# Optimization experiments

Hardware: AMD Instinct MI355X
Metric: run time of the kernel (lower is better)

## Reference

```python
import jax, jax.numpy as jnp
import numpy as np

N = 50000
E = 1600000
H = 64  # hidden_dim
NEG_SLOPE = 0.2  # PyG GATConv default


def _gat(x, src, dst, W, a_s, a_d, b, n):
    """Single-head PyG GATConv (heads=1, concat=True, add_self_loops applied by caller)."""
    h = x @ W                                   # [N, d_out]
    e = jax.nn.leaky_relu(h[src] @ a_s + h[dst] @ a_d, NEG_SLOPE)  # [E']
    # segment softmax over edges grouped by destination node
    m = jax.ops.segment_max(e, dst, num_segments=n)                # [N]
    ex = jnp.exp(e - m[dst])
    denom = jax.ops.segment_sum(ex, dst, num_segments=n)           # [N]
    alpha = ex / denom[dst]                                        # [E']
    out = jax.ops.segment_sum(alpha[:, None] * h[src], dst, num_segments=n)
    return out + b


def setup_inputs() -> dict:
    key = jax.random.key(0)
    ks = jax.random.split(key, 16)
    x = jax.random.normal(ks[0], (N, 1), jnp.float32)
    edge_index = jax.random.randint(ks[1], (2, E), 0, N, dtype=jnp.int32)
    edge_attr = jax.random.normal(ks[2], (E, 1), jnp.float32)  # unused by module

    def lin(k, fi, fo):
        return jax.random.normal(k, (fi, fo), jnp.float32) * (1.0 / np.sqrt(fi))

    def att(k, fo):
        return jax.random.normal(k, (fo,), jnp.float32) * (1.0 / np.sqrt(fo))

    return {
        "x": x, "edge_index": edge_index, "edge_attr": edge_attr,
        "W1": lin(ks[3], 1, H),  "as1": att(ks[4], H),  "ad1": att(ks[5], H),  "b1": jnp.zeros((H,), jnp.float32),
        "W2": lin(ks[6], H, H),  "as2": att(ks[7], H),  "ad2": att(ks[8], H),  "b2": jnp.zeros((H,), jnp.float32),
        "W3": lin(ks[9], H, 1),  "as3": att(ks[10], 1), "ad3": att(ks[11], 1), "b3": jnp.zeros((1,), jnp.float32),
    }


def reference(x, edge_index, edge_attr, W1, as1, ad1, b1, W2, as2, ad2, b2, W3, as3, ad3, b3):
    n = x.shape[0]
    # GATConv default add_self_loops=True
    loops = jnp.arange(n, dtype=edge_index.dtype)
    src = jnp.concatenate([edge_index[0], loops])
    dst = jnp.concatenate([edge_index[1], loops])
    h = jax.nn.relu(_gat(x, src, dst, W1, as1, ad1, b1, n))
    h = jax.nn.relu(_gat(h, src, dst, W2, as2, ad2, b2, n))
    out = _gat(h, src, dst, W3, as3, ad3, b3, n)
    return out.squeeze(-1)  # [N]
```

## Files before the change

### kernel.cpp

```cpp
#include <hip/hip_runtime.h>

#define NEG_SLOPE 0.2f
#define BSH 8
#define BSZ 256
#define SC_PT 16
#define SC_CHUNK (256 * SC_PT)
#define STAGE_MAX 24576
#define GH 256

__device__ __forceinline__ float leaky(float v) { return v > 0.f ? v : NEG_SLOPE * v; }
__device__ __forceinline__ float rdlane(float v, int l) {
    return __uint_as_float(__builtin_amdgcn_readlane(__float_as_uint(v), l));
}


__global__ void k_bhist(const int* __restrict__ dst, int E, int* __restrict__ parts) {
    __shared__ int h[256];
    int tid = threadIdx.x;
    h[tid] = 0;
    __syncthreads();
    for (int i = blockIdx.x * 256 + tid; i < E; i += GH * 256)
        atomicAdd(&h[dst[i] >> BSH], 1);
    __syncthreads();
    parts[(blockIdx.x << 8) | tid] = h[tid];
}

__global__ void k_bscan_prep(const int* __restrict__ parts, int NB,
                             int* __restrict__ bbase, int* __restrict__ bcursor,
                             const float* __restrict__ W1, const float* __restrict__ as1,
                             const float* __restrict__ ad1, const float* __restrict__ b1,
                             const float* __restrict__ W2, const float* __restrict__ as2,
                             const float* __restrict__ ad2, float* __restrict__ consts) {
    __shared__ int wsum[4];
    __shared__ float ts[64];
    int tid = threadIdx.x, lane = tid & 63, wid = tid >> 6;
    int v = 0;
    #pragma unroll
    for (int b = 0; b < GH; b++) v += parts[(b << 8) | tid];
    int s = v;
    #pragma unroll
    for (int off = 1; off < 64; off <<= 1) { int t = __shfl_up(s, off); if (lane >= off) s += t; }
    if (lane == 63) wsum[wid] = s;
    __syncthreads();
    int woff = 0;
    for (int w = 0; w < wid; w++) woff += wsum[w];
    int incl = woff + s;
    if (tid == 0) bbase[0] = 0;
    if (tid < NB) { bbase[tid + 1] = incl; bcursor[tid] = incl - v; }

    if (tid < 64) {
        float a = 0.f, b = 0.f, u = 0.f, vv = 0.f;
        for (int j = 0; j < 64; j++) {
            float w = W2[tid * 64 + j];
            a += w * as2[j];
            b += w * ad2[j];
            float w1f = W1[j];
            float w2c = W2[j * 64 + tid];
            if (w1f > 0.f) u += w2c * w1f;
            else if (w1f < 0.f) vv += w2c * w1f;
        }
        consts[2 + tid] = a;
        consts[66 + tid] = b;
        consts[322 + tid] = u;
        consts[386 + tid] = vv;
        float w1 = W1[tid];
        float r_cs = w1 * as1[tid];
        float r_cd = w1 * ad1[tid];
        float r_pa = (w1 > 0.f) ? w1 * a : 0.f;
        float r_na = (w1 < 0.f) ? w1 * a : 0.f;
        float r_pb = (w1 > 0.f) ? w1 * b : 0.f;
        float r_nb = (w1 < 0.f) ? w1 * b : 0.f;
        #pragma unroll
        for (int off = 32; off; off >>= 1) {
            r_cs += __shfl_xor(r_cs, off);
            r_cd += __shfl_xor(r_cd, off);
            r_pa += __shfl_xor(r_pa, off);
            r_na += __shfl_xor(r_na, off);
            r_pb += __shfl_xor(r_pb, off);
            r_nb += __shfl_xor(r_nb, off);
        }
        if (tid == 0) {
            consts[0] = r_cs;  consts[1] = r_cd;
            consts[451] = r_pa; consts[452] = r_na;
            consts[453] = r_pb; consts[454] = r_nb;
        }
        unsigned long long m = __ballot(b1[tid] == 0.f);
        if (tid == 0) consts[450] = (m == ~0ULL) ? 1.f : 0.f;
        float t = (w1 != 0.f) ? (-b1[tid] / w1) : 1e30f;
        ts[tid] = t;
        __builtin_amdgcn_s_barrier();
        int r = 0;
        for (int k = 0; k < 64; k++) {
            float tk = ts[k];
            r += (tk < t) || (tk == t && k < tid);
        }
        consts[130 + r] = t;
        consts[194 + tid] = (float)r;
        consts[258 + tid] = (w1 > 0.f) ? 1.f : (w1 < 0.f ? -1.f : 0.f);
    }
}

__global__ void k_bscatter(const int* __restrict__ src, const int* __restrict__ dst,
                           int E, int NB, int* __restrict__ bcursor,
                           unsigned int* __restrict__ bentry) {
    __shared__ int h[256], base[256], lcur[256];
    int tid = threadIdx.x;
    int b0 = blockIdx.x * SC_CHUNK;
    for (int i = tid; i < 256; i += 256) { h[i] = 0; lcur[i] = 0; }
    __syncthreads();
    int d[SC_PT], s[SC_PT];
    #pragma unroll
    for (int k = 0; k < SC_PT; k++) {
        int i = b0 + k * 256 + tid;
        if (i < E) { d[k] = dst[i]; s[k] = src[i]; atomicAdd(&h[d[k] >> BSH], 1); }
        else d[k] = -1;
    }
    __syncthreads();
    if (tid < NB && h[tid]) base[tid] = atomicAdd(&bcursor[tid], h[tid]);
    __syncthreads();
    #pragma unroll
    for (int k = 0; k < SC_PT; k++) {
        if (d[k] >= 0) {
            int b = d[k] >> BSH;
            int l = atomicAdd(&lcur[b], 1);
            bentry[base[b] + l] = ((unsigned)s[k] << BSH) | (unsigned)(d[k] & (BSZ - 1));
        }
    }
}

__global__ void k_build(const unsigned int* __restrict__ bentry, const int* __restrict__ bbase,
                        int N, int NB, int Etot,
                        int* __restrict__ rowptr, unsigned short* __restrict__ csr) {
    __shared__ int deg[256], lcur[256];
    __shared__ int wsum[4];
    __shared__ unsigned short stage[STAGE_MAX];
    int b = blockIdx.x, tid = threadIdx.x, lane = tid & 63, wid = tid >> 6;
    int node0 = b << BSH;
    int nvalid = min(256, N - node0);
    int ebeg = bbase[b], cnt = bbase[b + 1] - ebeg;
    deg[tid] = (tid < nvalid) ? 1 : 0;
    __syncthreads();
    for (int i = tid; i < cnt; i += 256)
        atomicAdd(&deg[bentry[ebeg + i] & (BSZ - 1)], 1);
    __syncthreads();
    int v = deg[tid], s = v;
    #pragma unroll
    for (int off = 1; off < 64; off <<= 1) { int t = __shfl_up(s, off); if (lane >= off) s += t; }
    if (lane == 63) wsum[wid] = s;
    __syncthreads();
    int woff = 0;
    for (int w = 0; w < wid; w++) woff += wsum[w];
    int excl = woff + s - v;
    int gstart = ebeg + node0;
    if (tid < nvalid) rowptr[node0 + tid] = gstart + excl;
    if (b == NB - 1 && tid == 0) rowptr[N] = Etot;
    if (tid < nvalid) { stage[excl] = (unsigned short)(node0 + tid); lcur[tid] = excl + 1; }
    else lcur[tid] = excl;
    __syncthreads();
    for (int i = tid; i < cnt; i += 256) {
        unsigned int e = bentry[ebeg + i];
        int pos = atomicAdd(&lcur[e & (BSZ - 1)], 1);
        stage[pos] = (unsigned short)(e >> BSH);
    }
    __syncthreads();
    int total = cnt + nvalid;
    for (int i = tid; i < total; i += 256) csr[gstart + i] = stage[i];
}

__global__ __launch_bounds__(256) void k_l1(
        const float* __restrict__ x, const int* __restrict__ rowptr,
        const unsigned short* __restrict__ csr, const float* __restrict__ consts,
        const float* __restrict__ W1, const float* __restrict__ b1,
        float2* __restrict__ sa2, float* __restrict__ d2, int N) {
    int w = (blockIdx.x * blockDim.x + threadIdx.x) >> 6;
    int lane = threadIdx.x & 63;
    int hl = lane & 31, half = lane >> 5;
    int n = w * 2 + half;
    if (w * 2 >= N) return;
    int nn = min(n, N - 1);
    float cs = consts[0], cd = consts[1];
    float xn = x[nn];
    float dn = xn * cd;
    float mself = leaky(fmaf(xn, cs, dn));
    int beg = rowptr[nn], end = rowptr[nn + 1];
    float den = 0.f, num = 0.f;
    for (int e = beg + hl; e < end; e += 32) {
        float v = x[csr[e]];
        float wt = __expf(leaky(fmaf(v, cs, dn)) - mself);
        den += wt;
        num = fmaf(wt, v, num);
    }
    #pragma unroll
    for (int off = 16; off; off >>= 1) {
        den += __shfl_xor(den, off);
        num += __shfl_xor(num, off);
    }
    float agg = num / den;

    if (consts[450] != 0.f) {
        if (hl == 0 && n < N) {
            float s2v = agg * (agg > 0.f ? consts[451] : consts[452]);
            float d2v = agg * (agg > 0.f ? consts[453] : consts[454]);
            sa2[n] = make_float2(s2v, agg);
            d2[n] = d2v;
        }
        return;
    }

    float aggA = rdlane(agg, 0), aggB = rdlane(agg, 32);
    float w1l = W1[lane], b1l = b1[lane];
    float ca = consts[2 + lane], cb = consts[66 + lane];
    #pragma unroll
    for (int q = 0; q < 2; q++) {
        float aq = q ? aggB : aggA;
        float t = fmaxf(fmaf(aq, w1l, b1l), 0.f);
        float a = t * ca, b = t * cb;
        #pragma unroll
        for (int off = 32; off; off >>= 1) {
            a += __shfl_xor(a, off);
            b += __shfl_xor(b, off);
        }
        int nq = w * 2 + q;
        if (lane == 0 && nq < N) { sa2[nq] = make_float2(a, aq); d2[nq] = b; }
    }
}

__global__ __launch_bounds__(256) void k_l2(
        const float2* __restrict__ sa2, const float* __restrict__ d2v,
        const int* __restrict__ rowptr, const unsigned short* __restrict__ csr,
        const float* __restrict__ consts,
        const float* __restrict__ W1, const float* __restrict__ b1,
        const float* __restrict__ W2, const float* __restrict__ b2,
        const float* __restrict__ W3,
        float* __restrict__ h3, int N) {
    __shared__ float Ts[64];
    __shared__ float bk0[4][66], bk1[4][66];
    __shared__ float accs[4][64];
    int tid = threadIdx.x, lane = tid & 63, wid = tid >> 6;

    if (consts[450] != 0.f) {
        int n0 = blockIdx.x * 8;
        if (n0 >= N) return;
        int hl = lane & 31, half = lane >> 5;
        int n = n0 + wid * 2 + half;
        int nn = min(n, N - 1);
        float dn = d2v[nn];
        float mx = leaky(sa2[nn].x + dn);
        int beg = rowptr[nn], end = rowptr[nn + 1];
        float T0 = 0.f, S1p = 0.f, S1n = 0.f;
        for (int e = beg + hl; e < end; e += 32) {
            float2 f2 = sa2[csr[e]];
            float w = __expf(leaky(f2.x + dn) - mx);
            T0 += w;
            float wav = w * f2.y;
            if (f2.y > 0.f) S1p += wav; else S1n += wav;
        }
        #pragma unroll
        for (int off = 16; off; off >>= 1) {
            T0 += __shfl_xor(T0, off);
            S1p += __shfl_xor(S1p, off);
            S1n += __shfl_xor(S1n, off);
        }
        float sp = S1p / T0, sn = S1n / T0;
        float spA = rdlane(sp, 0), snA = rdlane(sn, 0);
        float spB = rdlane(sp, 32), snB = rdlane(sn, 32);
        float uj = consts[322 + lane], vj = consts[386 + lane];
        float b2j = b2[lane], w3j = W3[lane];
        float oA = fmaf(uj, spA, fmaf(vj, snA, b2j));
        float oB = fmaf(uj, spB, fmaf(vj, snB, b2j));
        float cA = fmaxf(oA, 0.f) * w3j;
        float cB = fmaxf(oB, 0.f) * w3j;
        #pragma unroll
        for (int off = 32; off; off >>= 1) {
            cA += __shfl_xor(cA, off);
            cB += __shfl_xor(cB, off);
        }
        if (lane == 0) {
            int a = n0 + wid * 2;
            if (a < N) h3[a] = cA;
            if (a + 1 < N) h3[a + 1] = cB;
        }
        return;
    }

    if (tid < 64) Ts[tid] = consts[130 + tid];
    __syncthreads();
    int n0 = blockIdx.x * 4;
    int n = n0 + wid;
    bool act = (n < N);
    float acc = 0.f;
    if (act) {
        float w1l = W1[lane], b1l = b1[lane];
        int   rk  = (int)consts[194 + lane];
        float sg  = consts[258 + lane];
        float dn  = d2v[n];
        float mx  = leaky(sa2[n].x + dn);
        int beg = rowptr[n], end = rowptr[n + 1];
        bk0[wid][lane] = 0.f; bk1[wid][lane] = 0.f;
        if (lane == 0) { bk0[wid][64] = 0.f; bk1[wid][64] = 0.f; }
        __asm__ volatile("" ::: "memory");
        for (int e = beg + lane; e < end; e += 64) {
            float2 f2 = sa2[csr[e]];
            float w = __expf(leaky(f2.x + dn) - mx);
            float av = f2.y;
            int p = 0;
            #pragma unroll
            for (int step = 32; step; step >>= 1)
                if (Ts[p + step - 1] < av) p += step;
            atomicAdd(&bk0[wid][p], w);
            atomicAdd(&bk1[wid][p], w * av);
        }
        __asm__ volatile("" ::: "memory");
        float p0 = bk0[wid][lane], p1 = bk1[wid][lane];
        #pragma unroll
        for (int off = 1; off < 64; off <<= 1) {
            float t0 = __shfl_up(p0, off), t1 = __shfl_up(p1, off);
            if (lane >= off) { p0 += t0; p1 += t1; }
        }
        float T0 = rdlane(p0, 63) + bk0[wid][64];
        float T1 = rdlane(p1, 63) + bk1[wid][64];
        float P0r = __shfl(p0, rk), P1r = __shfl(p1, rk);
        if (sg > 0.f)      acc = fmaf(w1l, T1 - P1r, b1l * (T0 - P0r));
        else if (sg < 0.f) acc = fmaf(w1l, P1r, b1l * P0r);
        else               acc = fmaxf(b1l, 0.f) * T0;
        acc /= T0;
    }
    accs[wid][lane] = acc;
    __syncthreads();
    if (wid == 0) {
        float a0 = accs[0][lane], a1 = accs[1][lane];
        float a2 = accs[2][lane], a3 = accs[3][lane];
        float ob = b2[lane];
        float o0 = ob, o1 = ob, o2 = ob, o3 = ob;
        #pragma unroll 8
        for (int f = 0; f < 64; f++) {
            float w2 = W2[f * 64 + lane];
            o0 = fmaf(rdlane(a0, f), w2, o0);
            o1 = fmaf(rdlane(a1, f), w2, o1);
            o2 = fmaf(rdlane(a2, f), w2, o2);
            o3 = fmaf(rdlane(a3, f), w2, o3);
        }
        float w3 = W3[lane];
        float c0 = fmaxf(o0, 0.f) * w3, c1 = fmaxf(o1, 0.f) * w3;
        float c2 = fmaxf(o2, 0.f) * w3, c3 = fmaxf(o3, 0.f) * w3;
        #pragma unroll
        for (int off = 32; off; off >>= 1) {
            c0 += __shfl_xor(c0, off);
            c1 += __shfl_xor(c1, off);
            c2 += __shfl_xor(c2, off);
            c3 += __shfl_xor(c3, off);
        }
        if (lane < 4) {
            float cv = (lane == 0) ? c0 : (lane == 1) ? c1 : (lane == 2) ? c2 : c3;
            int nn2 = n0 + lane;
            if (nn2 < N) h3[nn2] = cv;
        }
    }
}

__global__ __launch_bounds__(256) void k_l3(
        const float* __restrict__ val, const int* __restrict__ rowptr,
        const unsigned short* __restrict__ csr,
        const float* __restrict__ cs_p, const float* __restrict__ cd_p,
        const float* __restrict__ bias, float* __restrict__ out, int N) {
    int w = (blockIdx.x * blockDim.x + threadIdx.x) >> 6;
    int lane = threadIdx.x & 63;
    int hl = lane & 31, half = lane >> 5;
    int n = w * 2 + half;
    if (w * 2 >= N) return;
    int nn = min(n, N - 1);
    float cs = cs_p[0], cd = cd_p[0];
    float vn = val[nn];
    float dn = vn * cd;
    float mself = leaky(fmaf(vn, cs, dn));
    int beg = rowptr[nn], end = rowptr[nn + 1];
    float den = 0.f, num = 0.f;
    for (int e = beg + hl; e < end; e += 32) {
        float v = val[csr[e]];
        float wt = __expf(leaky(fmaf(v, cs, dn)) - mself);
        den += wt;
        num = fmaf(wt, v, num);
    }
    #pragma unroll
    for (int off = 16; off; off >>= 1) {
        den += __shfl_xor(den, off);
        num += __shfl_xor(num, off);
    }
    if (hl == 0 && n < N) out[n] = num / den + bias[0];
}


extern "C" void kernel_launch(void* const* d_in, const int* in_sizes, int n_in,
                              void* d_out, int out_size, void* d_ws, size_t ws_size,
                              hipStream_t stream) {
    const int N = in_sizes[0];
    const int E = in_sizes[1] / 2;
    const int Etot = E + N;
    const int NB = (N + BSZ - 1) >> BSH;

    const float* x   = (const float*)d_in[0];
    const int*   ei  = (const int*)d_in[1];
    const int*   src = ei;
    const int*   dst = ei + E;
    const float* W1  = (const float*)d_in[3];
    const float* as1 = (const float*)d_in[4];
    const float* ad1 = (const float*)d_in[5];
    const float* b1  = (const float*)d_in[6];
    const float* W2  = (const float*)d_in[7];
    const float* as2 = (const float*)d_in[8];
    const float* ad2 = (const float*)d_in[9];
    const float* b2  = (const float*)d_in[10];
    const float* W3  = (const float*)d_in[11];
    const float* as3 = (const float*)d_in[12];
    const float* ad3 = (const float*)d_in[13];
    const float* b3  = (const float*)d_in[14];
    float* out = (float*)d_out;

    char* p = (char*)d_ws;
    auto alloc = [&](size_t bytes) {
        char* r = p;
        p += (bytes + 255) & ~(size_t)255;
        return r;
    };
    int*   parts   = (int*)alloc((size_t)GH * 256 * 4);
    int*   bbase   = (int*)alloc(257 * 4);
    int*   bcursor = (int*)alloc(256 * 4);
    int*   rowptr  = (int*)alloc((size_t)(N + 1) * 4);
    float* consts  = (float*)alloc(455 * sizeof(float));
    unsigned int*   bentry = (unsigned int*)alloc((size_t)E * 4);
    unsigned short* csr    = (unsigned short*)alloc((size_t)Etot * 2);
    float2* sa2    = (float2*)alloc((size_t)N * 8);
    float* d2      = (float*)alloc((size_t)N * 4);
    float* h3      = (float*)alloc((size_t)N * 4);

    const int B = 256;
    int gS  = (E + SC_CHUNK - 1) / SC_CHUNK;
    int nw2 = (N + 1) / 2;
    int gW2 = (int)(((size_t)nw2 * 64 + B - 1) / B);
    int gL2 = (N + 3) / 4;

    hipLaunchKernelGGL(k_bhist,      dim3(GH), dim3(B), 0, stream, dst, E, parts);
    hipLaunchKernelGGL(k_bscan_prep, dim3(1),  dim3(B), 0, stream, parts, NB, bbase, bcursor,
                       W1, as1, ad1, b1, W2, as2, ad2, consts);
    hipLaunchKernelGGL(k_bscatter,   dim3(gS), dim3(B), 0, stream, src, dst, E, NB, bcursor, bentry);
    hipLaunchKernelGGL(k_build,      dim3(NB), dim3(B), 0, stream, bentry, bbase, N, NB, Etot, rowptr, csr);

    hipLaunchKernelGGL(k_l1, dim3(gW2), dim3(B), 0, stream,
                       x, rowptr, csr, consts, W1, b1, sa2, d2, N);
    hipLaunchKernelGGL(k_l2, dim3(gL2), dim3(B), 0, stream,
                       sa2, d2, rowptr, csr, consts, W1, b1, W2, b2, W3, h3, N);
    hipLaunchKernelGGL(k_l3, dim3(gW2), dim3(B), 0, stream,
                       h3, rowptr, csr, as3, ad3, b3, out, N);
}
```

Before: 189.5 us.

## Fuse layer-1 aggregation into CSR build using staged neighbor lists in LDS

When the fast path flag consts[450] is set, layer-1 softmax aggregation is computed inside k_build, one thread per destination node. It reads neighbor indices from the shared-memory stage buffer, so the CSR does not have to be re-read from global memory and the k_l1 pass is skipped. The old k_l1 kernel becomes k_l1g, which returns early in that case but is still launched. The trade-off is that each thread now walks a whole node's neighbor list serially (about 32 edges), where before 32 lanes shared one node, so k_build does more serial work per thread.

Result: no change. 191.5 us (+1.1%).

```diff
diff --git a/kernel.cpp b/kernel.cpp
--- a/kernel.cpp
+++ b/kernel.cpp
@@ -130,7 +130,9 @@
 
 __global__ void k_build(const unsigned int* __restrict__ bentry, const int* __restrict__ bbase,
                         int N, int NB, int Etot,
-                        int* __restrict__ rowptr, unsigned short* __restrict__ csr) {
+                        const float* __restrict__ x, const float* __restrict__ consts,
+                        int* __restrict__ rowptr, unsigned short* __restrict__ csr,
+                        float2* __restrict__ sa2, float* __restrict__ d2) {
     __shared__ int deg[256], lcur[256];
     __shared__ int wsum[4];
     __shared__ unsigned short stage[STAGE_MAX];
@@ -165,13 +167,35 @@
     __syncthreads();
     int total = cnt + nvalid;
     for (int i = tid; i < total; i += 256) csr[gstart + i] = stage[i];
-}
-
-__global__ __launch_bounds__(256) void k_l1(
+
+    if (consts[450] != 0.f && tid < nvalid) {
+        int node = node0 + tid;
+        float cs = consts[0], cd = consts[1];
+        float xn = x[node];
+        float dn = xn * cd;
+        float mself = leaky(fmaf(xn, cs, dn));
+        float den = 0.f, num = 0.f;
+        int lbeg = excl, lend = excl + v;
+        for (int i = lbeg; i < lend; i++) {
+            float xv = x[stage[i]];
+            float wt = __expf(leaky(fmaf(xv, cs, dn)) - mself);
+            den += wt;
+            num = fmaf(wt, xv, num);
+        }
+        float agg = num / den;
+        float s2v = agg * (agg > 0.f ? consts[451] : consts[452]);
+        float d2v = agg * (agg > 0.f ? consts[453] : consts[454]);
+        sa2[node] = make_float2(s2v, agg);
+        d2[node] = d2v;
+    }
+}
+
+__global__ __launch_bounds__(256) void k_l1g(
         const float* __restrict__ x, const int* __restrict__ rowptr,
         const unsigned short* __restrict__ csr, const float* __restrict__ consts,
         const float* __restrict__ W1, const float* __restrict__ b1,
         float2* __restrict__ sa2, float* __restrict__ d2, int N) {
+    if (consts[450] != 0.f) return;
     int w = (blockIdx.x * blockDim.x + threadIdx.x) >> 6;
     int lane = threadIdx.x & 63;
     int hl = lane & 31, half = lane >> 5;
@@ -196,17 +220,6 @@
         num += __shfl_xor(num, off);
     }
     float agg = num / den;
-
-    if (consts[450] != 0.f) {
-        if (hl == 0 && n < N) {
-            float s2v = agg * (agg > 0.f ? consts[451] : consts[452]);
-            float d2v = agg * (agg > 0.f ? consts[453] : consts[454]);
-            sa2[n] = make_float2(s2v, agg);
-            d2[n] = d2v;
-        }
-        return;
-    }
-
     float aggA = rdlane(agg, 0), aggB = rdlane(agg, 32);
     float w1l = W1[lane], b1l = b1[lane];
     float ca = consts[2 + lane], cb = consts[66 + lane];
@@ -443,9 +456,10 @@
     hipLaunchKernelGGL(k_bscan_prep, dim3(1),  dim3(B), 0, stream, parts, NB, bbase, bcursor,
                        W1, as1, ad1, b1, W2, as2, ad2, consts);
     hipLaunchKernelGGL(k_bscatter,   dim3(gS), dim3(B), 0, stream, src, dst, E, NB, bcursor, bentry);
-    hipLaunchKernelGGL(k_build,      dim3(NB), dim3(B), 0, stream, bentry, bbase, N, NB, Etot, rowptr, csr);
-
-    hipLaunchKernelGGL(k_l1, dim3(gW2), dim3(B), 0, stream,
+    hipLaunchKernelGGL(k_build,      dim3(NB), dim3(B), 0, stream, bentry, bbase, N, NB, Etot,
+                       x, consts, rowptr, csr, sa2, d2);
+
+    hipLaunchKernelGGL(k_l1g, dim3(gW2), dim3(B), 0, stream,
                        x, rowptr, csr, consts, W1, b1, sa2, d2, N);
     hipLaunchKernelGGL(k_l2, dim3(gL2), dim3(B), 0, stream,
                        sa2, d2, rowptr, csr, consts, W1, b1, W2, b2, W3, h3, N);
```
